# Optimization experiments

Measured on AMD Instinct MI355X. Metric: run time of the kernel, lower is better.

The kernel has to match this reference:

```python
import jax, jax.numpy as jnp
import numpy as np

GROUP_SIZE = 128
IN_FEATURES = 4096
OUT_FEATURES = 11008
BATCH = 16


def setup_inputs() -> dict:
    key = jax.random.key(0)
    k_x, k_q, k_s, k_z, k_b = jax.random.split(key, 5)
    num_groups = IN_FEATURES // GROUP_SIZE
    x = jax.random.normal(k_x, (BATCH, IN_FEATURES), dtype=jnp.float32)
    # packed int4 pairs stored as bytes in [0, 256)
    qweight = jax.random.randint(k_q, (OUT_FEATURES, IN_FEATURES // 2), 0, 256, dtype=jnp.int32)
    # positive scales of realistic magnitude, zeros in [0, 15]
    scales = jax.random.uniform(k_s, (OUT_FEATURES, num_groups), dtype=jnp.float32) * 0.01 + 1e-4
    zeros = jax.random.uniform(k_z, (OUT_FEATURES, num_groups), dtype=jnp.float32) * 15.0
    bias = jax.random.normal(k_b, (OUT_FEATURES,), dtype=jnp.float32)
    return {"x": x, "qweight": qweight, "scales": scales, "zeros": zeros, "bias": bias}


def _unpack_int4(packed, in_features):
    # packed: [O, I//2] ints in [0,256); low nibble is even column, high nibble odd
    low = packed & 15
    high = (packed >> 4) & 15
    return jnp.stack([low, high], axis=-1).reshape(packed.shape[0], in_features)  # [O, I]


def reference(x, qweight, scales, zeros, bias):
    q = _unpack_int4(qweight, IN_FEATURES).astype(jnp.float32)        # [O, I]
    s = jnp.repeat(scales, GROUP_SIZE, axis=1)                        # [O, I]
    z = jnp.repeat(zeros, GROUP_SIZE, axis=1)                         # [O, I]
    w = (q - z) * s                                                   # dequantized weight [O, I]
    return x @ w.T + bias                                             # [B, O]
```

## Files before the change

kernel.cpp:

```cpp
#include <hip/hip_runtime.h>
#include <hip/hip_fp16.h>

#define IN_F   4096
#define OUT_F  11008
#define BATCH  16
#define GROUPS 32
#define PPR    2048

typedef __attribute__((ext_vector_type(8))) _Float16 half8;
typedef __attribute__((ext_vector_type(2))) _Float16 h2;
typedef __attribute__((ext_vector_type(4))) float    float4_t;
typedef __attribute__((ext_vector_type(4))) int      int4_t;
typedef __attribute__((ext_vector_type(4))) unsigned uint4_t;

__device__ inline h2 cvt2(float a, float b) {
    return __builtin_bit_cast(h2, __builtin_amdgcn_cvt_pkrtz(a, b));
}

#define GLOAD_LDS(srcp, ldsp) \
    __builtin_amdgcn_global_load_lds( \
        (const __attribute__((address_space(1))) void*)(srcp), \
        (__attribute__((address_space(3))) void*)(ldsp), 16, 0, 0)

__global__ __launch_bounds__(256) void xcvt_perm(const float* __restrict__ x,
                                                 _Float16* __restrict__ xp) {
    const int T = blockIdx.x * 256 + threadIdx.x;
    const int step = T >> 6, lane = T & 63;
    const int b = lane & 15, k = step * 32 + (lane >> 4) * 8;
    const float4_t a0 = *(const float4_t*)(x + b * IN_F + k);
    const float4_t a1 = *(const float4_t*)(x + b * IN_F + k + 4);
    half8 h;
    h2 p0 = cvt2(a0.x, a0.y), p1 = cvt2(a0.z, a0.w);
    h2 p2 = cvt2(a1.x, a1.y), p3 = cvt2(a1.z, a1.w);
    h[0]=p0[0]; h[1]=p0[1]; h[2]=p1[0]; h[3]=p1[1];
    h[4]=p2[0]; h[5]=p2[1]; h[6]=p3[0]; h[7]=p3[1];
    *(half8*)(xp + step * 512 + lane * 8) = h;
}

__global__ __launch_bounds__(256, 4) void gptq_gemm_full(
    const _Float16* __restrict__ xp, const int* __restrict__ qw,
    const float* __restrict__ scales, const float* __restrict__ zeros,
    const float* __restrict__ bias, float* __restrict__ out)
{
    __shared__ int   lq[2][16 * 256];
    __shared__ float red[4][16][17];

    const int tid  = threadIdx.x;
    const int lane = tid & 63, wave = tid >> 6;
    const int otile = blockIdx.x;
    const int ln = lane & 15, lk = lane >> 4;
    const int o  = otile * 16 + ln;
    const int x3 = ln & 7;

    h2 s2g[8], c2g[8];
    #pragma unroll
    for (int c = 0; c < 8; ++c) {
        const float s = scales[o * GROUPS + c * 4 + wave];
        const float z = zeros [o * GROUPS + c * 4 + wave];
        s2g[c] = cvt2(s, s);
        c2g[c] = cvt2(-z * s, -z * s);
    }
    const h2 k1024 = { (_Float16)1024.0f, (_Float16)1024.0f };

    asm volatile("s_waitcnt vmcnt(0)" ::: "memory");
    __builtin_amdgcn_sched_barrier(0);

    half8 xv[2][4];
    float4_t acc = {0.f, 0.f, 0.f, 0.f};

#define STAGE(C, BUF) { \
    _Pragma("unroll") \
    for (int i = 0; i < 4; ++i) { \
        const int row = wave * 4 + i; \
        const int* s0 = qw + (otile * 16 + row) * PPR + (C) * 256 \
                      + ((lane ^ (row & 7)) * 4); \
        GLOAD_LDS(s0, &lq[BUF][row * 256]); \
    } \
    __builtin_amdgcn_sched_barrier(0); }

#define XLOAD(C, BUF) { \
    const char* xc = (const char*)xp + ((C) * 16 + wave * 4) * 1024 + lane * 16; \
    asm volatile("global_load_dwordx4 %0, %1, off"             : "=v"(xv[BUF][0]) : "v"(xc)); \
    asm volatile("global_load_dwordx4 %0, %1, off offset:1024" : "=v"(xv[BUF][1]) : "v"(xc)); \
    asm volatile("global_load_dwordx4 %0, %1, off offset:2048" : "=v"(xv[BUF][2]) : "v"(xc)); \
    asm volatile("global_load_dwordx4 %0, %1, off offset:3072" : "=v"(xv[BUF][3]) : "v"(xc)); \
    __builtin_amdgcn_sched_barrier(0); }

#define WAITV8 { asm volatile("s_waitcnt vmcnt(8)" ::: "memory"); \
                 __builtin_amdgcn_sched_barrier(0); }
#define WAITV0 { asm volatile("s_waitcnt vmcnt(0)" ::: "memory"); \
                 __builtin_amdgcn_sched_barrier(0); }
#define BARR   { __builtin_amdgcn_s_barrier(); \
                 __builtin_amdgcn_sched_barrier(0); }

#define COMPUTE(C, BUF) { \
    _Pragma("unroll") \
    for (int t = 0; t < 4; ++t) { \
        const int4_t v = *(const int4_t*)((const char*)lq + (BUF) * 16384 \
            + ln * 1024 + (((wave * 16 + t * 4 + lk) ^ x3) << 4)); \
        uint4_t bw; \
        _Pragma("unroll") \
        for (int i = 0; i < 4; ++i) { \
            const unsigned pv = (unsigned)v[i]; \
            const unsigned u = (pv & 0xFu) | ((pv << 12) & 0xF0000u) \
                             | 0x64006400u;             \
            h2 q = __builtin_bit_cast(h2, u) - k1024;   \
            h2 w = q * s2g[C] + c2g[C];                 \
            bw[i] = __builtin_bit_cast(unsigned, w); \
        } \
        acc = __builtin_amdgcn_mfma_f32_16x16x32_f16( \
            xv[BUF][t], __builtin_bit_cast(half8, bw), acc, 0, 0, 0); \
    } }

    STAGE(0, 0) XLOAD(0, 0)
    STAGE(1, 1) XLOAD(1, 1)

    WAITV8 BARR COMPUTE(0, 0) BARR STAGE(2, 0) XLOAD(2, 0)
    WAITV8 BARR COMPUTE(1, 1) BARR STAGE(3, 1) XLOAD(3, 1)
    WAITV8 BARR COMPUTE(2, 0) BARR STAGE(4, 0) XLOAD(4, 0)
    WAITV8 BARR COMPUTE(3, 1) BARR STAGE(5, 1) XLOAD(5, 1)
    WAITV8 BARR COMPUTE(4, 0) BARR STAGE(6, 0) XLOAD(6, 0)
    WAITV8 BARR COMPUTE(5, 1) BARR STAGE(7, 1) XLOAD(7, 1)
    WAITV8 BARR COMPUTE(6, 0) BARR
    WAITV0 BARR COMPUTE(7, 1)

#undef STAGE
#undef XLOAD
#undef WAITV8
#undef WAITV0
#undef BARR
#undef COMPUTE

    #pragma unroll
    for (int r = 0; r < 4; ++r) red[wave][lk * 4 + r][ln] = acc[r];
    __syncthreads();

    const int row = tid >> 4, col = tid & 15;
    const float sum = red[0][row][col] + red[1][row][col]
                    + red[2][row][col] + red[3][row][col];
    const int oo = otile * 16 + col;
    out[row * OUT_F + oo] = sum + bias[oo];
}

__global__ __launch_bounds__(256) void gptq_gemm_fb(
    const float* __restrict__ x, const int* __restrict__ qw,
    const float* __restrict__ scales, const float* __restrict__ zeros,
    const float* __restrict__ bias, float* __restrict__ out)
{
    const int tid  = threadIdx.x;
    const int lane = tid & 63;
    const int wave = tid >> 6;
    const int otile = blockIdx.x;
    const int ln = lane & 15, lk = lane >> 4;
    const int o = otile * 16 + ln;
    const int kc0 = wave * 1024;

    const int* qbase = qw + o * PPR + (kc0 >> 1) + lk * 4;
    const float* srow = scales + o * GROUPS;
    const float* zrow = zeros  + o * GROUPS;

    float4_t acc = {0.f, 0.f, 0.f, 0.f};
    const h2 k1024 = { (_Float16)1024.0f, (_Float16)1024.0f };

    #pragma unroll
    for (int ch = 0; ch < 4; ++ch) {
        const int cc = kc0 + ch * 256;
        h2 s2[2], c2[2];
        #pragma unroll
        for (int gi = 0; gi < 2; ++gi) {
            const float s  = srow[(cc >> 7) + gi];
            const float c0 = -zrow[(cc >> 7) + gi] * s;
            s2[gi] = cvt2(s, s); c2[gi] = cvt2(c0, c0);
        }
        #pragma unroll
        for (int t = 0; t < 8; ++t) {
            const int4_t v = *(const int4_t*)(qbase + ch * 128 + t * 16);
            const float* xq = x + ln * IN_F + cc + t * 32 + lk * 8;
            const float4_t a0 = *(const float4_t*)(xq);
            const float4_t a1 = *(const float4_t*)(xq + 4);
            half8 af;
            h2 p0 = cvt2(a0.x, a0.y), p1 = cvt2(a0.z, a0.w);
            h2 p2 = cvt2(a1.x, a1.y), p3 = cvt2(a1.z, a1.w);
            af[0]=p0[0]; af[1]=p0[1]; af[2]=p1[0]; af[3]=p1[1];
            af[4]=p2[0]; af[5]=p2[1]; af[6]=p3[0]; af[7]=p3[1];
            const int gi = t >> 2;
            uint4_t bw;
            #pragma unroll
            for (int i = 0; i < 4; ++i) {
                const unsigned pv = (unsigned)v[i];
                const unsigned u = (pv & 0xFu) | ((pv << 12) & 0xF0000u)
                                 | 0x64006400u;
                h2 q = __builtin_bit_cast(h2, u) - k1024;
                h2 w = q * s2[gi] + c2[gi];
                bw[i] = __builtin_bit_cast(unsigned, w);
            }
            acc = __builtin_amdgcn_mfma_f32_16x16x32_f16(
                af, __builtin_bit_cast(half8, bw), acc, 0, 0, 0);
        }
    }

    __shared__ float red[4][16][17];
    #pragma unroll
    for (int r = 0; r < 4; ++r) red[wave][lk * 4 + r][ln] = acc[r];
    __syncthreads();
    const int row = tid >> 4, col = tid & 15;
    const float sum = red[0][row][col] + red[1][row][col]
                    + red[2][row][col] + red[3][row][col];
    const int oo = otile * 16 + col;
    out[row * OUT_F + oo] = sum + bias[oo];
}

extern "C" void kernel_launch(void* const* d_in, const int* in_sizes, int n_in,
                              void* d_out, int out_size, void* d_ws, size_t ws_size,
                              hipStream_t stream) {
    const float* x      = (const float*)d_in[0];
    const int*   qwgt   = (const int*)d_in[1];
    const float* scales = (const float*)d_in[2];
    const float* zeros  = (const float*)d_in[3];
    const float* bias   = (const float*)d_in[4];
    float* out = (float*)d_out;

    const int nOTiles = OUT_F / 16;

    if (d_ws && ws_size >= (size_t)(1 << 20)) {
        _Float16* xp = (_Float16*)d_ws;
        hipLaunchKernelGGL(xcvt_perm, dim3(32), dim3(256), 0, stream, x, xp);
        hipLaunchKernelGGL(gptq_gemm_full, dim3(nOTiles), dim3(256), 0, stream,
                           xp, qwgt, scales, zeros, bias, out);
    } else {
        hipLaunchKernelGGL(gptq_gemm_fb, dim3(nOTiles), dim3(256), 0, stream,
                           x, qwgt, scales, zeros, bias, out);
    }
}
```

Before: 31.04 us.

## Split K across eight waves per block and reuse staging LDS for reduction

Doubles the block to 512 threads so each of eight waves handles half as many K-steps per chunk. This halves per-wave weight staging, x loads and MFMA work, and raises the number of waves in flight to hide memory latency. The cross-wave reduction reuses the weight staging buffer instead of a separate array, and the LDS swizzle now XORs with the full 4-bit row index. The cost is an eight-way reduction and higher register and occupancy pressure under the launch bound of 512 threads with 8 blocks.

```diff
diff --git a/kernel.cpp b/kernel.cpp
--- a/kernel.cpp
+++ b/kernel.cpp
@@ -37,26 +37,25 @@
     *(half8*)(xp + step * 512 + lane * 8) = h;
 }
 
-__global__ __launch_bounds__(256, 4) void gptq_gemm_full(
+__global__ __launch_bounds__(512, 8) void gptq_gemm_full(
     const _Float16* __restrict__ xp, const int* __restrict__ qw,
     const float* __restrict__ scales, const float* __restrict__ zeros,
     const float* __restrict__ bias, float* __restrict__ out)
 {
-    __shared__ int   lq[2][16 * 256];
-    __shared__ float red[4][16][17];
+    __shared__ int lq[2][16 * 256];
 
     const int tid  = threadIdx.x;
     const int lane = tid & 63, wave = tid >> 6;
     const int otile = blockIdx.x;
     const int ln = lane & 15, lk = lane >> 4;
     const int o  = otile * 16 + ln;
-    const int x3 = ln & 7;
 
     h2 s2g[8], c2g[8];
     #pragma unroll
     for (int c = 0; c < 8; ++c) {
-        const float s = scales[o * GROUPS + c * 4 + wave];
-        const float z = zeros [o * GROUPS + c * 4 + wave];
+        const int g = c * 4 + (wave >> 1);
+        const float s = scales[o * GROUPS + g];
+        const float z = zeros [o * GROUPS + g];
         s2g[c] = cvt2(s, s);
         c2g[c] = cvt2(-z * s, -z * s);
     }
@@ -65,81 +64,85 @@
     asm volatile("s_waitcnt vmcnt(0)" ::: "memory");
     __builtin_amdgcn_sched_barrier(0);
 
-    half8 xv[2][4];
+    half8 xvA0, xvA1, xvB0, xvB1;
     float4_t acc = {0.f, 0.f, 0.f, 0.f};
 
 #define STAGE(C, BUF) { \
     _Pragma("unroll") \
-    for (int i = 0; i < 4; ++i) { \
-        const int row = wave * 4 + i; \
-        const int* s0 = qw + (otile * 16 + row) * PPR + (C) * 256 \
-                      + ((lane ^ (row & 7)) * 4); \
-        GLOAD_LDS(s0, &lq[BUF][row * 256]); \
+    for (int i = 0; i < 2; ++i) { \
+        const int r = wave * 2 + i; \
+        const int* src = qw + (otile * 16 + r) * PPR + (C) * 256 \
+                       + ((lane ^ r) * 4); \
+        GLOAD_LDS(src, &lq[BUF][r * 256]); \
     } \
     __builtin_amdgcn_sched_barrier(0); }
 
-#define XLOAD(C, BUF) { \
-    const char* xc = (const char*)xp + ((C) * 16 + wave * 4) * 1024 + lane * 16; \
-    asm volatile("global_load_dwordx4 %0, %1, off"             : "=v"(xv[BUF][0]) : "v"(xc)); \
-    asm volatile("global_load_dwordx4 %0, %1, off offset:1024" : "=v"(xv[BUF][1]) : "v"(xc)); \
-    asm volatile("global_load_dwordx4 %0, %1, off offset:2048" : "=v"(xv[BUF][2]) : "v"(xc)); \
-    asm volatile("global_load_dwordx4 %0, %1, off offset:3072" : "=v"(xv[BUF][3]) : "v"(xc)); \
+#define XLOAD(C, N0, N1) { \
+    const char* xc = (const char*)xp + ((C) * 16 + wave * 2) * 1024 + lane * 16; \
+    asm volatile("global_load_dwordx4 %0, %1, off"             : "=v"(N0) : "v"(xc)); \
+    asm volatile("global_load_dwordx4 %0, %1, off offset:1024" : "=v"(N1) : "v"(xc)); \
     __builtin_amdgcn_sched_barrier(0); }
 
-#define WAITV8 { asm volatile("s_waitcnt vmcnt(8)" ::: "memory"); \
+#define WAITV4 { asm volatile("s_waitcnt vmcnt(4)" ::: "memory"); \
                  __builtin_amdgcn_sched_barrier(0); }
 #define WAITV0 { asm volatile("s_waitcnt vmcnt(0)" ::: "memory"); \
                  __builtin_amdgcn_sched_barrier(0); }
 #define BARR   { __builtin_amdgcn_s_barrier(); \
                  __builtin_amdgcn_sched_barrier(0); }
 
-#define COMPUTE(C, BUF) { \
+#define STEP(C, BUF, T, XF) { \
+    const int4_t v = *(const int4_t*)((const char*)lq + (BUF) * 16384 \
+        + ln * 1024 + (((wave * 8 + (T) * 4 + lk) ^ ln) << 4)); \
+    uint4_t bw; \
     _Pragma("unroll") \
-    for (int t = 0; t < 4; ++t) { \
-        const int4_t v = *(const int4_t*)((const char*)lq + (BUF) * 16384 \
-            + ln * 1024 + (((wave * 16 + t * 4 + lk) ^ x3) << 4)); \
-        uint4_t bw; \
-        _Pragma("unroll") \
-        for (int i = 0; i < 4; ++i) { \
-            const unsigned pv = (unsigned)v[i]; \
-            const unsigned u = (pv & 0xFu) | ((pv << 12) & 0xF0000u) \
-                             | 0x64006400u;             \
-            h2 q = __builtin_bit_cast(h2, u) - k1024;   \
-            h2 w = q * s2g[C] + c2g[C];                 \
-            bw[i] = __builtin_bit_cast(unsigned, w); \
-        } \
-        acc = __builtin_amdgcn_mfma_f32_16x16x32_f16( \
-            xv[BUF][t], __builtin_bit_cast(half8, bw), acc, 0, 0, 0); \
-    } }
-
-    STAGE(0, 0) XLOAD(0, 0)
-    STAGE(1, 1) XLOAD(1, 1)
-
-    WAITV8 BARR COMPUTE(0, 0) BARR STAGE(2, 0) XLOAD(2, 0)
-    WAITV8 BARR COMPUTE(1, 1) BARR STAGE(3, 1) XLOAD(3, 1)
-    WAITV8 BARR COMPUTE(2, 0) BARR STAGE(4, 0) XLOAD(4, 0)
-    WAITV8 BARR COMPUTE(3, 1) BARR STAGE(5, 1) XLOAD(5, 1)
-    WAITV8 BARR COMPUTE(4, 0) BARR STAGE(6, 0) XLOAD(6, 0)
-    WAITV8 BARR COMPUTE(5, 1) BARR STAGE(7, 1) XLOAD(7, 1)
-    WAITV8 BARR COMPUTE(6, 0) BARR
-    WAITV0 BARR COMPUTE(7, 1)
+    for (int i = 0; i < 4; ++i) { \
+        const unsigned pv = (unsigned)v[i]; \
+        const unsigned u = (pv & 0xFu) | ((pv << 12) & 0xF0000u) \
+                         | 0x64006400u;             \
+        h2 q = __builtin_bit_cast(h2, u) - k1024;   \
+        h2 w = q * s2g[C] + c2g[C];                 \
+        bw[i] = __builtin_bit_cast(unsigned, w); \
+    } \
+    acc = __builtin_amdgcn_mfma_f32_16x16x32_f16( \
+        (XF), __builtin_bit_cast(half8, bw), acc, 0, 0, 0); }
+
+#define COMPA(C) { STEP(C, 0, 0, xvA0) STEP(C, 0, 1, xvA1) }
+#define COMPB(C) { STEP(C, 1, 0, xvB0) STEP(C, 1, 1, xvB1) }
+
+    STAGE(0, 0) XLOAD(0, xvA0, xvA1)
+    STAGE(1, 1) XLOAD(1, xvB0, xvB1)
+
+    WAITV4 BARR COMPA(0) BARR STAGE(2, 0) XLOAD(2, xvA0, xvA1)
+    WAITV4 BARR COMPB(1) BARR STAGE(3, 1) XLOAD(3, xvB0, xvB1)
+    WAITV4 BARR COMPA(2) BARR STAGE(4, 0) XLOAD(4, xvA0, xvA1)
+    WAITV4 BARR COMPB(3) BARR STAGE(5, 1) XLOAD(5, xvB0, xvB1)
+    WAITV4 BARR COMPA(4) BARR STAGE(6, 0) XLOAD(6, xvA0, xvA1)
+    WAITV4 BARR COMPB(5) BARR STAGE(7, 1) XLOAD(7, xvB0, xvB1)
+    WAITV4 BARR COMPA(6) BARR
+    WAITV0 BARR COMPB(7)
 
 #undef STAGE
 #undef XLOAD
-#undef WAITV8
+#undef WAITV4
 #undef WAITV0
 #undef BARR
-#undef COMPUTE
-
-    #pragma unroll
-    for (int r = 0; r < 4; ++r) red[wave][lk * 4 + r][ln] = acc[r];
+#undef STEP
+#undef COMPA
+#undef COMPB
+
+    float* red = (float*)lq;
+    #pragma unroll
+    for (int r = 0; r < 4; ++r)
+        red[wave * 272 + (lk * 4 + r) * 17 + ln] = acc[r];
     __syncthreads();
 
-    const int row = tid >> 4, col = tid & 15;
-    const float sum = red[0][row][col] + red[1][row][col]
-                    + red[2][row][col] + red[3][row][col];
-    const int oo = otile * 16 + col;
-    out[row * OUT_F + oo] = sum + bias[oo];
+    if (tid < 256) {
+        const int row = tid >> 4, col = tid & 15;
+        float s = bias[otile * 16 + col];
+        #pragma unroll
+        for (int w = 0; w < 8; ++w) s += red[w * 272 + row * 17 + col];
+        out[row * OUT_F + otile * 16 + col] = s;
+    }
 }
 
 __global__ __launch_bounds__(256) void gptq_gemm_fb(
@@ -225,7 +228,7 @@
     if (d_ws && ws_size >= (size_t)(1 << 20)) {
         _Float16* xp = (_Float16*)d_ws;
         hipLaunchKernelGGL(xcvt_perm, dim3(32), dim3(256), 0, stream, x, xp);
-        hipLaunchKernelGGL(gptq_gemm_full, dim3(nOTiles), dim3(256), 0, stream,
+        hipLaunchKernelGGL(gptq_gemm_full, dim3(nOTiles), dim3(512), 0, stream,
                            xp, qwgt, scales, zeros, bias, out);
     } else {
         hipLaunchKernelGGL(gptq_gemm_fb, dim3(nOTiles), dim3(256), 0, stream,
```

Result: slower. 33.49 us (+7.9%).

## Fuse x fp32-to-fp16 conversion into GEMM and drop separate pre-pass kernel

Applied to the files above, without the earlier changes.

Removes the separate xcvt_perm launch that converted and permuted x to fp16 in workspace. The main kernel now loads fp32 x directly (eight dwordx4 loads per stage instead of four) and converts to fp16 inside the compute loop. The weight LDS loads gain a non-temporal cache hint, and launch bounds drop to 2 waves per EU to leave room for the larger register footprint. This saves one kernel launch and a global round trip, at the cost of doubled x traffic per block, extra conversion ALU work in the inner loop, and possibly lower occupancy.

```diff
diff --git a/kernel.cpp b/kernel.cpp
--- a/kernel.cpp
+++ b/kernel.cpp
@@ -17,28 +17,13 @@
     return __builtin_bit_cast(h2, __builtin_amdgcn_cvt_pkrtz(a, b));
 }
 
-#define GLOAD_LDS(srcp, ldsp) \
+#define GLOAD_LDS_NT(srcp, ldsp) \
     __builtin_amdgcn_global_load_lds( \
         (const __attribute__((address_space(1))) void*)(srcp), \
-        (__attribute__((address_space(3))) void*)(ldsp), 16, 0, 0)
+        (__attribute__((address_space(3))) void*)(ldsp), 16, 0, 2)
 
-__global__ __launch_bounds__(256) void xcvt_perm(const float* __restrict__ x,
-                                                 _Float16* __restrict__ xp) {
-    const int T = blockIdx.x * 256 + threadIdx.x;
-    const int step = T >> 6, lane = T & 63;
-    const int b = lane & 15, k = step * 32 + (lane >> 4) * 8;
-    const float4_t a0 = *(const float4_t*)(x + b * IN_F + k);
-    const float4_t a1 = *(const float4_t*)(x + b * IN_F + k + 4);
-    half8 h;
-    h2 p0 = cvt2(a0.x, a0.y), p1 = cvt2(a0.z, a0.w);
-    h2 p2 = cvt2(a1.x, a1.y), p3 = cvt2(a1.z, a1.w);
-    h[0]=p0[0]; h[1]=p0[1]; h[2]=p1[0]; h[3]=p1[1];
-    h[4]=p2[0]; h[5]=p2[1]; h[6]=p3[0]; h[7]=p3[1];
-    *(half8*)(xp + step * 512 + lane * 8) = h;
-}
-
-__global__ __launch_bounds__(256, 4) void gptq_gemm_full(
-    const _Float16* __restrict__ xp, const int* __restrict__ qw,
+__global__ __launch_bounds__(256, 2) void gptq_gemm_full(
+    const float* __restrict__ x, const int* __restrict__ qw,
     const float* __restrict__ scales, const float* __restrict__ zeros,
     const float* __restrict__ bias, float* __restrict__ out)
 {
@@ -65,39 +50,50 @@
     asm volatile("s_waitcnt vmcnt(0)" ::: "memory");
     __builtin_amdgcn_sched_barrier(0);
 
-    half8 xv[2][4];
+    float4_t xf[2][8];
     float4_t acc = {0.f, 0.f, 0.f, 0.f};
 
 #define STAGE(C, BUF) { \
     _Pragma("unroll") \
     for (int i = 0; i < 4; ++i) { \
-        const int row = wave * 4 + i; \
-        const int* s0 = qw + (otile * 16 + row) * PPR + (C) * 256 \
-                      + ((lane ^ (row & 7)) * 4); \
-        GLOAD_LDS(s0, &lq[BUF][row * 256]); \
+        const int r = wave * 4 + i; \
+        const int* src = qw + (otile * 16 + r) * PPR + (C) * 256 \
+                       + ((lane ^ (r & 7)) * 4); \
+        GLOAD_LDS_NT(src, &lq[BUF][r * 256]); \
     } \
     __builtin_amdgcn_sched_barrier(0); }
 
 #define XLOAD(C, BUF) { \
-    const char* xc = (const char*)xp + ((C) * 16 + wave * 4) * 1024 + lane * 16; \
-    asm volatile("global_load_dwordx4 %0, %1, off"             : "=v"(xv[BUF][0]) : "v"(xc)); \
-    asm volatile("global_load_dwordx4 %0, %1, off offset:1024" : "=v"(xv[BUF][1]) : "v"(xc)); \
-    asm volatile("global_load_dwordx4 %0, %1, off offset:2048" : "=v"(xv[BUF][2]) : "v"(xc)); \
-    asm volatile("global_load_dwordx4 %0, %1, off offset:3072" : "=v"(xv[BUF][3]) : "v"(xc)); \
+    const char* xc = (const char*)x \
+        + ((ln * IN_F + (C) * 512 + wave * 128 + lk * 8) << 2); \
+    asm volatile("global_load_dwordx4 %0, %1, off"            : "=v"(xf[BUF][0]) : "v"(xc)); \
+    asm volatile("global_load_dwordx4 %0, %1, off offset:16"  : "=v"(xf[BUF][1]) : "v"(xc)); \
+    asm volatile("global_load_dwordx4 %0, %1, off offset:128" : "=v"(xf[BUF][2]) : "v"(xc)); \
+    asm volatile("global_load_dwordx4 %0, %1, off offset:144" : "=v"(xf[BUF][3]) : "v"(xc)); \
+    asm volatile("global_load_dwordx4 %0, %1, off offset:256" : "=v"(xf[BUF][4]) : "v"(xc)); \
+    asm volatile("global_load_dwordx4 %0, %1, off offset:272" : "=v"(xf[BUF][5]) : "v"(xc)); \
+    asm volatile("global_load_dwordx4 %0, %1, off offset:384" : "=v"(xf[BUF][6]) : "v"(xc)); \
+    asm volatile("global_load_dwordx4 %0, %1, off offset:400" : "=v"(xf[BUF][7]) : "v"(xc)); \
     __builtin_amdgcn_sched_barrier(0); }
 
-#define WAITV8 { asm volatile("s_waitcnt vmcnt(8)" ::: "memory"); \
-                 __builtin_amdgcn_sched_barrier(0); }
-#define WAITV0 { asm volatile("s_waitcnt vmcnt(0)" ::: "memory"); \
-                 __builtin_amdgcn_sched_barrier(0); }
-#define BARR   { __builtin_amdgcn_s_barrier(); \
-                 __builtin_amdgcn_sched_barrier(0); }
+#define WAITV12 { asm volatile("s_waitcnt vmcnt(12)" ::: "memory"); \
+                  __builtin_amdgcn_sched_barrier(0); }
+#define WAITV0  { asm volatile("s_waitcnt vmcnt(0)"  ::: "memory"); \
+                  __builtin_amdgcn_sched_barrier(0); }
+#define BARR    { __builtin_amdgcn_s_barrier(); \
+                  __builtin_amdgcn_sched_barrier(0); }
 
 #define COMPUTE(C, BUF) { \
     _Pragma("unroll") \
     for (int t = 0; t < 4; ++t) { \
         const int4_t v = *(const int4_t*)((const char*)lq + (BUF) * 16384 \
             + ln * 1024 + (((wave * 16 + t * 4 + lk) ^ x3) << 4)); \
+        const float4_t a0 = xf[BUF][t * 2], a1 = xf[BUF][t * 2 + 1]; \
+        half8 af; \
+        { h2 p0 = cvt2(a0.x, a0.y), p1 = cvt2(a0.z, a0.w); \
+          h2 p2 = cvt2(a1.x, a1.y), p3 = cvt2(a1.z, a1.w); \
+          af[0]=p0[0]; af[1]=p0[1]; af[2]=p1[0]; af[3]=p1[1]; \
+          af[4]=p2[0]; af[5]=p2[1]; af[6]=p3[0]; af[7]=p3[1]; } \
         uint4_t bw; \
         _Pragma("unroll") \
         for (int i = 0; i < 4; ++i) { \
@@ -109,24 +105,24 @@
             bw[i] = __builtin_bit_cast(unsigned, w); \
         } \
         acc = __builtin_amdgcn_mfma_f32_16x16x32_f16( \
-            xv[BUF][t], __builtin_bit_cast(half8, bw), acc, 0, 0, 0); \
+            af, __builtin_bit_cast(half8, bw), acc, 0, 0, 0); \
     } }
 
     STAGE(0, 0) XLOAD(0, 0)
     STAGE(1, 1) XLOAD(1, 1)
 
-    WAITV8 BARR COMPUTE(0, 0) BARR STAGE(2, 0) XLOAD(2, 0)
-    WAITV8 BARR COMPUTE(1, 1) BARR STAGE(3, 1) XLOAD(3, 1)
-    WAITV8 BARR COMPUTE(2, 0) BARR STAGE(4, 0) XLOAD(4, 0)
-    WAITV8 BARR COMPUTE(3, 1) BARR STAGE(5, 1) XLOAD(5, 1)
-    WAITV8 BARR COMPUTE(4, 0) BARR STAGE(6, 0) XLOAD(6, 0)
-    WAITV8 BARR COMPUTE(5, 1) BARR STAGE(7, 1) XLOAD(7, 1)
-    WAITV8 BARR COMPUTE(6, 0) BARR
-    WAITV0 BARR COMPUTE(7, 1)
+    WAITV12 BARR COMPUTE(0, 0) BARR STAGE(2, 0) XLOAD(2, 0)
+    WAITV12 BARR COMPUTE(1, 1) BARR STAGE(3, 1) XLOAD(3, 1)
+    WAITV12 BARR COMPUTE(2, 0) BARR STAGE(4, 0) XLOAD(4, 0)
+    WAITV12 BARR COMPUTE(3, 1) BARR STAGE(5, 1) XLOAD(5, 1)
+    WAITV12 BARR COMPUTE(4, 0) BARR STAGE(6, 0) XLOAD(6, 0)
+    WAITV12 BARR COMPUTE(5, 1) BARR STAGE(7, 1) XLOAD(7, 1)
+    WAITV12 BARR COMPUTE(6, 0) BARR
+    WAITV0  BARR COMPUTE(7, 1)
 
 #undef STAGE
 #undef XLOAD
-#undef WAITV8
+#undef WAITV12
 #undef WAITV0
 #undef BARR
 #undef COMPUTE
@@ -135,74 +131,6 @@
     for (int r = 0; r < 4; ++r) red[wave][lk * 4 + r][ln] = acc[r];
     __syncthreads();
 
-    const int row = tid >> 4, col = tid & 15;
-    const float sum = red[0][row][col] + red[1][row][col]
-                    + red[2][row][col] + red[3][row][col];
-    const int oo = otile * 16 + col;
-    out[row * OUT_F + oo] = sum + bias[oo];
-}
-
-__global__ __launch_bounds__(256) void gptq_gemm_fb(
-    const float* __restrict__ x, const int* __restrict__ qw,
-    const float* __restrict__ scales, const float* __restrict__ zeros,
-    const float* __restrict__ bias, float* __restrict__ out)
-{
-    const int tid  = threadIdx.x;
-    const int lane = tid & 63;
-    const int wave = tid >> 6;
-    const int otile = blockIdx.x;
-    const int ln = lane & 15, lk = lane >> 4;
-    const int o = otile * 16 + ln;
-    const int kc0 = wave * 1024;
-
-    const int* qbase = qw + o * PPR + (kc0 >> 1) + lk * 4;
-    const float* srow = scales + o * GROUPS;
-    const float* zrow = zeros  + o * GROUPS;
-
-    float4_t acc = {0.f, 0.f, 0.f, 0.f};
-    const h2 k1024 = { (_Float16)1024.0f, (_Float16)1024.0f };
-
-    #pragma unroll
-    for (int ch = 0; ch < 4; ++ch) {
-        const int cc = kc0 + ch * 256;
-        h2 s2[2], c2[2];
-        #pragma unroll
-        for (int gi = 0; gi < 2; ++gi) {
-            const float s  = srow[(cc >> 7) + gi];
-            const float c0 = -zrow[(cc >> 7) + gi] * s;
-            s2[gi] = cvt2(s, s); c2[gi] = cvt2(c0, c0);
-        }
-        #pragma unroll
-        for (int t = 0; t < 8; ++t) {
-            const int4_t v = *(const int4_t*)(qbase + ch * 128 + t * 16);
-            const float* xq = x + ln * IN_F + cc + t * 32 + lk * 8;
-            const float4_t a0 = *(const float4_t*)(xq);
-            const float4_t a1 = *(const float4_t*)(xq + 4);
-            half8 af;
-            h2 p0 = cvt2(a0.x, a0.y), p1 = cvt2(a0.z, a0.w);
-            h2 p2 = cvt2(a1.x, a1.y), p3 = cvt2(a1.z, a1.w);
-            af[0]=p0[0]; af[1]=p0[1]; af[2]=p1[0]; af[3]=p1[1];
-            af[4]=p2[0]; af[5]=p2[1]; af[6]=p3[0]; af[7]=p3[1];
-            const int gi = t >> 2;
-            uint4_t bw;
-            #pragma unroll
-            for (int i = 0; i < 4; ++i) {
-                const unsigned pv = (unsigned)v[i];
-                const unsigned u = (pv & 0xFu) | ((pv << 12) & 0xF0000u)
-                                 | 0x64006400u;
-                h2 q = __builtin_bit_cast(h2, u) - k1024;
-                h2 w = q * s2[gi] + c2[gi];
-                bw[i] = __builtin_bit_cast(unsigned, w);
-            }
-            acc = __builtin_amdgcn_mfma_f32_16x16x32_f16(
-                af, __builtin_bit_cast(half8, bw), acc, 0, 0, 0);
-        }
-    }
-
-    __shared__ float red[4][16][17];
-    #pragma unroll
-    for (int r = 0; r < 4; ++r) red[wave][lk * 4 + r][ln] = acc[r];
-    __syncthreads();
     const int row = tid >> 4, col = tid & 15;
     const float sum = red[0][row][col] + red[1][row][col]
                     + red[2][row][col] + red[3][row][col];
@@ -220,15 +148,6 @@
     const float* bias   = (const float*)d_in[4];
     float* out = (float*)d_out;
 
-    const int nOTiles = OUT_F / 16;
-
-    if (d_ws && ws_size >= (size_t)(1 << 20)) {
-        _Float16* xp = (_Float16*)d_ws;
-        hipLaunchKernelGGL(xcvt_perm, dim3(32), dim3(256), 0, stream, x, xp);
-        hipLaunchKernelGGL(gptq_gemm_full, dim3(nOTiles), dim3(256), 0, stream,
-                           xp, qwgt, scales, zeros, bias, out);
-    } else {
-        hipLaunchKernelGGL(gptq_gemm_fb, dim3(nOTiles), dim3(256), 0, stream,
-                           x, qwgt, scales, zeros, bias, out);
-    }
+    hipLaunchKernelGGL(gptq_gemm_full, dim3(OUT_F / 16), dim3(256), 0, stream,
+                       x, qwgt, scales, zeros, bias, out);
 }
```

New measurement: 41.95 us. 1.35x slower.
